# Optimization experiments

Hardware: AMD Instinct MI355X
Metric: run time of the kernel (lower is better)

Reference implementation:

```python
import jax, jax.numpy as jnp
import numpy as np

B, S, D = 2, 2048, 1024
H = 16
HD = D // H  # 64


def setup_inputs() -> dict:
    key = jax.random.key(0)
    ks = jax.random.split(key, 6)
    x = jax.random.normal(ks[0], (B, S, D), dtype=jnp.float32)
    sc = 1.0 / np.sqrt(D)
    Wq = jax.random.normal(ks[1], (D, D), dtype=jnp.float32) * sc
    Wk = jax.random.normal(ks[2], (D, D), dtype=jnp.float32) * sc
    Wv = jax.random.normal(ks[3], (D, D), dtype=jnp.float32) * sc
    Wo = jax.random.normal(ks[4], (D, D), dtype=jnp.float32) * sc
    bo = jax.random.normal(ks[5], (D,), dtype=jnp.float32) * 0.01
    return {"x": x, "Wq": Wq, "Wk": Wk, "Wv": Wv, "Wo": Wo, "bo": bo}


def reference(x, Wq, Wk, Wv, Wo, bo):
    b, s, d = x.shape
    # projections (torch Linear: y = x @ W.T; weights here stored as [d_in, d_out])
    Q = (x @ Wq).reshape(b, s, H, HD).transpose(0, 2, 1, 3)  # [b,h,s,hd]
    K = (x @ Wk).reshape(b, s, H, HD).transpose(0, 2, 1, 3)
    V = (x @ Wv).reshape(b, s, H, HD).transpose(0, 2, 1, 3)
    scores = jnp.einsum("bhqd,bhkd->bhqk", Q, K) / np.sqrt(HD)
    causal = jnp.triu(jnp.ones((s, s), dtype=bool), k=1)  # True above diagonal
    scores = jnp.where(causal[None, None], -jnp.inf, scores)
    attn = jax.nn.softmax(scores, axis=-1)
    # dropout_rate = 0.0 -> identity (eval-mode reference)
    ctx = jnp.einsum("bhqk,bhkd->bhqd", attn, V)
    ctx = ctx.transpose(0, 2, 1, 3).reshape(b, s, d)
    return ctx @ Wo + bo
```

## Files before the change

kernel.cpp:

```cpp
#include <hip/hip_runtime.h>
#include <hip/hip_bf16.h>

#define B_  2
#define S_  2048
#define D_  1024
#define H_  16
#define HD_ 64
#define M_  (B_*S_)

typedef __attribute__((ext_vector_type(8))) short short8;
typedef __attribute__((ext_vector_type(4))) float f32x4;

#define MFMA16(a, b, c) __builtin_amdgcn_mfma_f32_16x16x32_bf16((a), (b), (c), 0, 0, 0)

static __device__ inline short f2bf(float f) {
    union { float f; unsigned u; } v; v.f = f;
    unsigned r = v.u + 0x7FFFu + ((v.u >> 16) & 1u);
    return (short)(r >> 16);
}

static __device__ __forceinline__ float fexp2(float x) {
    float r;
    asm volatile("v_exp_f32 %0, %1\n\ts_nop 1" : "=v"(r) : "v"(x));
    return r;
}

static __device__ __forceinline__ unsigned cvt_pk_bf16(float lo, float hi) {
    unsigned r;
    asm volatile("v_cvt_pk_bf16_f32 %0, %1, %2" : "=v"(r) : "v"(lo), "v"(hi));
    return r;
}

static __device__ __forceinline__ void gl_lds16(const short* g, short* l) {
    __builtin_amdgcn_global_load_lds(
        (const __attribute__((address_space(1))) void*)g,
        (__attribute__((address_space(3))) void*)l, 16, 0, 0);
}

__global__ void prep_kernel(const float* __restrict__ x,
                            const float* __restrict__ Wq, const float* __restrict__ Wk,
                            const float* __restrict__ Wv, const float* __restrict__ Wo,
                            short* __restrict__ xb,
                            short* __restrict__ Wqkvt, short* __restrict__ Wot) {
    int z = blockIdx.z;
    if (z == 4) {
        int bid = blockIdx.y * 32 + blockIdx.x;
        int base = bid * 1024 + threadIdx.x;
#pragma unroll
        for (int it = 0; it < 4; ++it) {
            int i = base + it * 256;
            float4 v = ((const float4*)x)[i];
            short4 o;
            o.x = f2bf(v.x); o.y = f2bf(v.y); o.z = f2bf(v.z); o.w = f2bf(v.w);
            ((short4*)xb)[i] = o;
        }
        return;
    }
    __shared__ float tile[32][33];
    const float* W = (z == 0) ? Wq : (z == 1) ? Wk : (z == 2) ? Wv : Wo;
    short* Wt = (z == 3) ? Wot : (Wqkvt + ((size_t)z << 20));
    int tx = threadIdx.x & 31, ty = threadIdx.x >> 5;
    int n0 = blockIdx.x * 32, k0 = blockIdx.y * 32;
#pragma unroll
    for (int i = 0; i < 4; ++i)
        tile[ty + 8 * i][tx] = W[(size_t)(k0 + ty + 8 * i) * D_ + n0 + tx];
    __syncthreads();
#pragma unroll
    for (int i = 0; i < 4; ++i)
        Wt[(size_t)(n0 + ty + 8 * i) * D_ + k0 + tx] = f2bf(tile[tx][ty + 8 * i]);
}

__global__ __launch_bounds__(256) void gemm_qkv(const short* __restrict__ A,
                                                const short* __restrict__ Bt,
                                                short* __restrict__ out) {
    __shared__ __align__(16) short Asm[2][128 * 32];
    __shared__ __align__(16) short Bsm[2][128 * 32];
    const int NBX = 3;
    int X = blockIdx.x & 7, t = blockIdx.x >> 3;
    int bm = t / NBX, bn = X * NBX + t % NBX;
    int tid = threadIdx.x, l = tid & 63, w = tid >> 6;
    int lhi = l >> 4, llo = l & 15;
    int wm = w >> 1, wn = w & 1;

    f32x4 acc[4][4];
#pragma unroll
    for (int m = 0; m < 4; ++m)
#pragma unroll
        for (int n = 0; n < 4; ++n) acc[m][n] = (f32x4){0.f, 0.f, 0.f, 0.f};

    const short* Ag = A + (size_t)(bm * 128) * 1024;
    const short* Bg = Bt + (size_t)(bn * 128) * 1024;
    int c0 = tid, c1 = 256 + tid;
    int r0 = ((c0 >> 5) << 3) | (c0 & 7), s0 = ((c0 >> 3) & 3) ^ (r0 & 3);
    int r1 = ((c1 >> 5) << 3) | (c1 & 7), s1 = ((c1 >> 3) & 3) ^ (r1 & 3);

    auto stage = [&](int buf, int k0) {
        gl_lds16(Ag + (size_t)r0 * 1024 + k0 + s0 * 8, &Asm[buf][c0 * 8]);
        gl_lds16(Ag + (size_t)r1 * 1024 + k0 + s1 * 8, &Asm[buf][c1 * 8]);
        gl_lds16(Bg + (size_t)r0 * 1024 + k0 + s0 * 8, &Bsm[buf][c0 * 8]);
        gl_lds16(Bg + (size_t)r1 * 1024 + k0 + s1 * 8, &Bsm[buf][c1 * 8]);
    };

    int cia[4], cib[4];
#pragma unroll
    for (int m = 0; m < 4; ++m) {
        int row = wm * 64 + m * 16 + llo;
        cia[m] = ((row >> 3) << 5) | (((lhi ^ row) & 3) << 3) | (row & 7);
    }
#pragma unroll
    for (int n = 0; n < 4; ++n) {
        int row = wn * 64 + n * 16 + llo;
        cib[n] = ((row >> 3) << 5) | (((lhi ^ row) & 3) << 3) | (row & 7);
    }

    stage(0, 0);
    for (int i = 0; i < 32; ++i) {
        asm volatile("s_waitcnt vmcnt(0)" ::: "memory");
        __builtin_amdgcn_s_barrier();
        asm volatile("" ::: "memory");
        if (i + 1 < 32) stage((i + 1) & 1, (i + 1) * 32);
        int cur = i & 1;
        short8 af[4], bf[4];
#pragma unroll
        for (int m = 0; m < 4; ++m) af[m] = *(const short8*)&Asm[cur][cia[m] * 8];
#pragma unroll
        for (int n = 0; n < 4; ++n) bf[n] = *(const short8*)&Bsm[cur][cib[n] * 8];
#pragma unroll
        for (int m = 0; m < 4; ++m)
#pragma unroll
            for (int n = 0; n < 4; ++n)
                acc[m][n] = MFMA16(af[m], bf[n], acc[m][n]);
    }

    int rowb = bm * 128 + wm * 64, colb = bn * 128 + wn * 64;
#pragma unroll
    for (int m = 0; m < 4; ++m) {
#pragma unroll
        for (int n = 0; n < 4; ++n) {
            int col = colb + n * 16 + llo;
#pragma unroll
            for (int j = 0; j < 4; ++j) {
                int row = rowb + m * 16 + lhi * 4 + j;
                float v = acc[m][n][j];
                int proj = col >> 10, n1 = col & 1023;
                int h = n1 >> 6, hd = n1 & 63;
                int b = row >> 11, s = row & 2047;
                size_t off;
                if (proj == 0)
                    off = ((size_t)(b * 16 + h) * 2048 + s) * 64 + hd;
                else if (proj == 1)
                    off = (size_t)M_ * D_ + ((size_t)(b * 16 + h) * 2048 + s) * 64 + hd;
                else
                    off = (size_t)2 * M_ * D_ + ((size_t)(b * 16 + h) * 64 + hd) * 2048 + s;
                out[off] = f2bf(v);
            }
        }
    }
}

__global__ __launch_bounds__(256, 6) void gemm_out(const short* __restrict__ A,
                                                   const short* __restrict__ Bt,
                                                   const float* __restrict__ bias,
                                                   float* __restrict__ out) {
    __shared__ __align__(16) short Asm[2][64 * 32];
    __shared__ __align__(16) short Bsm[2][128 * 32];
    int bn = blockIdx.x & 7, bm = blockIdx.x >> 3;
    int tid = threadIdx.x, l = tid & 63, w = tid >> 6;
    int lhi = l >> 4, llo = l & 15;

    f32x4 acc[4][2];
#pragma unroll
    for (int m = 0; m < 4; ++m)
#pragma unroll
        for (int n = 0; n < 2; ++n) acc[m][n] = (f32x4){0.f, 0.f, 0.f, 0.f};

    const short* Ag = A + (size_t)(bm * 64) * 1024;
    const short* Bg = Bt + (size_t)(bn * 128) * 1024;
    int ca = tid;
    int ra = ((ca >> 5) << 3) | (ca & 7), sa = ((ca >> 3) & 3) ^ (ra & 3);
    int cb0 = tid, cb1 = tid + 256;
    int rb0 = ((cb0 >> 5) << 3) | (cb0 & 7), sb0 = ((cb0 >> 3) & 3) ^ (rb0 & 3);
    int rb1 = ((cb1 >> 5) << 3) | (cb1 & 7), sb1 = ((cb1 >> 3) & 3) ^ (rb1 & 3);

    auto stage = [&](int buf, int k0) {
        gl_lds16(Ag + (size_t)ra * 1024 + k0 + sa * 8, &Asm[buf][ca * 8]);
        gl_lds16(Bg + (size_t)rb0 * 1024 + k0 + sb0 * 8, &Bsm[buf][cb0 * 8]);
        gl_lds16(Bg + (size_t)rb1 * 1024 + k0 + sb1 * 8, &Bsm[buf][cb1 * 8]);
    };

    int cia[4], cib[2];
#pragma unroll
    for (int m = 0; m < 4; ++m) {
        int row = m * 16 + llo;
        cia[m] = ((row >> 3) << 5) | (((lhi ^ row) & 3) << 3) | (row & 7);
    }
#pragma unroll
    for (int n = 0; n < 2; ++n) {
        int row = w * 32 + n * 16 + llo;
        cib[n] = ((row >> 3) << 5) | (((lhi ^ row) & 3) << 3) | (row & 7);
    }

    stage(0, 0);
    for (int i = 0; i < 32; ++i) {
        asm volatile("s_waitcnt vmcnt(0)" ::: "memory");
        __builtin_amdgcn_s_barrier();
        asm volatile("" ::: "memory");
        if (i + 1 < 32) stage((i + 1) & 1, (i + 1) * 32);
        int cur = i & 1;
        short8 af[4], bf[2];
#pragma unroll
        for (int m = 0; m < 4; ++m) af[m] = *(const short8*)&Asm[cur][cia[m] * 8];
#pragma unroll
        for (int n = 0; n < 2; ++n) bf[n] = *(const short8*)&Bsm[cur][cib[n] * 8];
#pragma unroll
        for (int m = 0; m < 4; ++m)
#pragma unroll
            for (int n = 0; n < 2; ++n)
                acc[m][n] = MFMA16(af[m], bf[n], acc[m][n]);
    }

    int rowb = bm * 64, colb = bn * 128 + w * 32;
#pragma unroll
    for (int m = 0; m < 4; ++m)
#pragma unroll
        for (int n = 0; n < 2; ++n) {
            int col = colb + n * 16 + llo;
#pragma unroll
            for (int j = 0; j < 4; ++j) {
                int row = rowb + m * 16 + lhi * 4 + j;
                out[(size_t)row * 1024 + col] = acc[m][n][j] + bias[col];
            }
        }
}

__global__ __launch_bounds__(512) void attn_kernel(const short* __restrict__ Q,
                                                   const short* __restrict__ Kg,
                                                   const short* __restrict__ Vt,
                                                   short* __restrict__ ctx) {
    __shared__ __align__(16) char kvbuf[2][16384];
    __shared__ __align__(16) char plds[8][2048];
    int tid = threadIdx.x, w = tid >> 6, l = tid & 63;
    int lhi = l >> 4, llo = l & 15;
    int bh = blockIdx.x & 31, qp = blockIdx.x >> 5;
    int b = bh >> 4, h = bh & 15;
    char* pb = plds[w];

    const short* Qh = Q + (size_t)bh * S_ * HD_;
    const short* Kh = Kg + (size_t)bh * S_ * HD_;
    const short* Vh = Vt + (size_t)bh * HD_ * S_;

    int qbA = qp, qbB = 15 - qp;
    int NTA = 2 * qp + 2;
    const int NT = 34;

    int srow = tid >> 3;
    int ssrc = (16 * (tid & 7)) ^ ((srow & 7) << 4);
    auto stage = [&](char* buf, int c0) {
        gl_lds16(Kh + (size_t)(c0 + srow) * HD_ + (ssrc >> 1), (short*)(buf + tid * 16));
        gl_lds16(Vh + (size_t)srow * S_ + c0 + (ssrc >> 1), (short*)(buf + 8192 + tid * 16));
    };

    f32x4 O[4];
#pragma unroll
    for (int n = 0; n < 4; ++n) O[n] = (f32x4){0.f, 0.f, 0.f, 0.f};
    float lpart[4] = {0.f, 0.f, 0.f, 0.f};

    auto writeOut = [&](int qb) {
        int qbs = qb * 128 + w * 16;
#pragma unroll
        for (int j = 0; j < 4; ++j) {
            float ls = lpart[j];
            ls += __shfl_xor(ls, 1);
            ls += __shfl_xor(ls, 2);
            ls += __shfl_xor(ls, 4);
            ls += __shfl_xor(ls, 8);
            float inv = 1.0f / ls;
            int row = qbs + lhi * 4 + j;
            size_t base = ((size_t)(b * S_ + row)) * D_ + h * HD_;
#pragma unroll
            for (int n = 0; n < 4; ++n)
                ctx[base + n * 16 + llo] = f2bf(O[n][j] * inv);
        }
    };

    const float SC = 0.18033688f;
    const float M2 = 17.312340f;

    int qbase = qbA * 128 + w * 16;
    short8 aq0 = *(const short8*)(Qh + (size_t)(qbase + llo) * HD_ + 8 * lhi);
    short8 aq1 = *(const short8*)(Qh + (size_t)(qbase + llo) * HD_ + 32 + 8 * lhi);

    stage(kvbuf[0], 0);

    for (int i = 0; i < NT; ++i) {
        asm volatile("s_waitcnt vmcnt(0)" ::: "memory");
        __builtin_amdgcn_s_barrier();
        asm volatile("" ::: "memory");
        int kt = (i < NTA) ? i : i - NTA;
        int c0 = kt * 64;
        if (i + 1 < NT) {
            int ni = i + 1;
            int nkt = (ni < NTA) ? ni : ni - NTA;
            stage(kvbuf[ni & 1], nkt * 64);
        }
        const char* kb = kvbuf[i & 1];
        const char* vb = kb + 8192;

        if (c0 <= qbase + 15) {
            f32x4 sc4[4];
#pragma unroll
            for (int cb = 0; cb < 4; ++cb) {
                int row = cb * 16 + llo;
                int sw = (row & 7) << 4;
                short8 kf0 = *(const short8*)(kb + row * 128 + ((16 * lhi) ^ sw));
                short8 kf1 = *(const short8*)(kb + row * 128 + ((64 + 16 * lhi) ^ sw));
                f32x4 z = (f32x4){0.f, 0.f, 0.f, 0.f};
                z = MFMA16(aq0, kf0, z);
                z = MFMA16(aq1, kf1, z);
                sc4[cb] = z;
            }
            bool diag = (c0 + 63 > qbase);
#pragma unroll
            for (int j = 0; j < 4; ++j) {
                int qr = qbase + lhi * 4 + j;
                float v0 = fmaf(sc4[0][j], SC, -M2);
                float v1 = fmaf(sc4[1][j], SC, -M2);
                float v2 = fmaf(sc4[2][j], SC, -M2);
                float v3 = fmaf(sc4[3][j], SC, -M2);
                if (diag) {
                    if (c0 + llo > qr)      v0 = -1e30f;
                    if (c0 + 16 + llo > qr) v1 = -1e30f;
                    if (c0 + 32 + llo > qr) v2 = -1e30f;
                    if (c0 + 48 + llo > qr) v3 = -1e30f;
                }
                float p0 = fexp2(v0), p1 = fexp2(v1);
                float p2 = fexp2(v2), p3 = fexp2(v3);
                lpart[j] += (p0 + p1) + (p2 + p3);
                unsigned pk01 = cvt_pk_bf16(p0, p1);
                unsigned pk23 = cvt_pk_bf16(p2, p3);
                int r = lhi * 4 + j;
                char* rb = pb + r * 128;
                int sw = (r & 7) << 4;
                *(short*)(rb + ((2 * llo) ^ sw))      = (short)(pk01);
                *(short*)(rb + ((2 * llo + 32) ^ sw)) = (short)(pk01 >> 16);
                *(short*)(rb + ((2 * llo + 64) ^ sw)) = (short)(pk23);
                *(short*)(rb + ((2 * llo + 96) ^ sw)) = (short)(pk23 >> 16);
            }
            int swr = (llo & 7) << 4;
            short8 pa0 = *(const short8*)(pb + llo * 128 + ((16 * lhi) ^ swr));
            short8 pa1 = *(const short8*)(pb + llo * 128 + ((64 + 16 * lhi) ^ swr));
#pragma unroll
            for (int n = 0; n < 4; ++n) {
                int row = n * 16 + llo;
                int sw = (row & 7) << 4;
                short8 vf0 = *(const short8*)(vb + row * 128 + ((16 * lhi) ^ sw));
                short8 vf1 = *(const short8*)(vb + row * 128 + ((64 + 16 * lhi) ^ sw));
                O[n] = MFMA16(pa0, vf0, O[n]);
                O[n] = MFMA16(pa1, vf1, O[n]);
            }
        }

        if (i == NTA - 1) {
            writeOut(qbA);
#pragma unroll
            for (int n = 0; n < 4; ++n) O[n] = (f32x4){0.f, 0.f, 0.f, 0.f};
            lpart[0] = lpart[1] = lpart[2] = lpart[3] = 0.f;
            qbase = qbB * 128 + w * 16;
            aq0 = *(const short8*)(Qh + (size_t)(qbase + llo) * HD_ + 8 * lhi);
            aq1 = *(const short8*)(Qh + (size_t)(qbase + llo) * HD_ + 32 + 8 * lhi);
        }
    }
    writeOut(qbB);
}

extern "C" void kernel_launch(void* const* d_in, const int* in_sizes, int n_in,
                              void* d_out, int out_size, void* d_ws, size_t ws_size,
                              hipStream_t stream) {
    const float* x  = (const float*)d_in[0];
    const float* Wq = (const float*)d_in[1];
    const float* Wk = (const float*)d_in[2];
    const float* Wv = (const float*)d_in[3];
    const float* Wo = (const float*)d_in[4];
    const float* bo = (const float*)d_in[5];
    float* out = (float*)d_out;

    char* ws = (char*)d_ws;
    short* xb    = (short*)(ws);
    short* Wqkvt = (short*)(ws + (size_t)(8 << 20));
    short* Wot   = (short*)(ws + (size_t)(14 << 20));
    short* Qb    = (short*)(ws + (size_t)(16 << 20));
    short* Kb    = Qb + (size_t)M_ * D_;
    short* Vtb   = Qb + (size_t)2 * M_ * D_;
    short* ctx   = xb;

    prep_kernel<<<dim3(32, 32, 5), 256, 0, stream>>>(x, Wq, Wk, Wv, Wo, xb, Wqkvt, Wot);
    gemm_qkv<<<768, 256, 0, stream>>>(xb, Wqkvt, Qb);
    attn_kernel<<<256, 512, 0, stream>>>(Qb, Kb, Vtb, ctx);
    gemm_out<<<512, 256, 0, stream>>>(ctx, Wot, bo, out);
}
```

Measured before the change: 133.8 us.

## Rewrite QKV GEMM as 256x256-tile 8-wave ping-pong pipelined kernel

The QKV projection GEMM now uses 256x256 output tiles with 512 threads (8 waves), BK=64 and an 8-way XOR swizzle. It loads in halves across double buffers with fine-grained barriers, so that LDS reads, global-to-LDS staging and MFMA work interleave within each K step. The aim is fewer blocks (192), each with more reuse of A and B, and better overlap of memory traffic with matrix math. In exchange, register pressure rises (128 accumulator floats per lane) and there are many more barriers per iteration, which can limit occupancy.

```diff
diff --git a/kernel.cpp b/kernel.cpp
--- a/kernel.cpp
+++ b/kernel.cpp
@@ -70,78 +70,145 @@
         Wt[(size_t)(n0 + ty + 8 * i) * D_ + k0 + tx] = f2bf(tile[tx][ty + 8 * i]);
 }
 
-__global__ __launch_bounds__(256) void gemm_qkv(const short* __restrict__ A,
-                                                const short* __restrict__ Bt,
-                                                short* __restrict__ out) {
-    __shared__ __align__(16) short Asm[2][128 * 32];
-    __shared__ __align__(16) short Bsm[2][128 * 32];
-    const int NBX = 3;
-    int X = blockIdx.x & 7, t = blockIdx.x >> 3;
-    int bm = t / NBX, bn = X * NBX + t % NBX;
+__global__ __launch_bounds__(512) void gemm_qkv8p(const short* __restrict__ A,
+                                                  const short* __restrict__ Bt,
+                                                  short* __restrict__ out) {
+    __shared__ __align__(16) short lds[2][2][2][8192];
+    int wg = (blockIdx.x & 7) * 24 + (blockIdx.x >> 3);
+    int bn = wg / 16, bm = wg % 16;
     int tid = threadIdx.x, l = tid & 63, w = tid >> 6;
     int lhi = l >> 4, llo = l & 15;
-    int wm = w >> 1, wn = w & 1;
-
-    f32x4 acc[4][4];
-#pragma unroll
-    for (int m = 0; m < 4; ++m)
+    int wm = w >> 2, wn = w & 3;
+    int bh = wn >> 1;
+
+    f32x4 acc[8][4];
+#pragma unroll
+    for (int m = 0; m < 8; ++m)
 #pragma unroll
         for (int n = 0; n < 4; ++n) acc[m][n] = (f32x4){0.f, 0.f, 0.f, 0.f};
 
-    const short* Ag = A + (size_t)(bm * 128) * 1024;
-    const short* Bg = Bt + (size_t)(bn * 128) * 1024;
-    int c0 = tid, c1 = 256 + tid;
-    int r0 = ((c0 >> 5) << 3) | (c0 & 7), s0 = ((c0 >> 3) & 3) ^ (r0 & 3);
-    int r1 = ((c1 >> 5) << 3) | (c1 & 7), s1 = ((c1 >> 3) & 3) ^ (r1 & 3);
-
-    auto stage = [&](int buf, int k0) {
-        gl_lds16(Ag + (size_t)r0 * 1024 + k0 + s0 * 8, &Asm[buf][c0 * 8]);
-        gl_lds16(Ag + (size_t)r1 * 1024 + k0 + s1 * 8, &Asm[buf][c1 * 8]);
-        gl_lds16(Bg + (size_t)r0 * 1024 + k0 + s0 * 8, &Bsm[buf][c0 * 8]);
-        gl_lds16(Bg + (size_t)r1 * 1024 + k0 + s1 * 8, &Bsm[buf][c1 * 8]);
-    };
-
-    int cia[4], cib[4];
-#pragma unroll
-    for (int m = 0; m < 4; ++m) {
-        int row = wm * 64 + m * 16 + llo;
-        cia[m] = ((row >> 3) << 5) | (((lhi ^ row) & 3) << 3) | (row & 7);
-    }
-#pragma unroll
-    for (int n = 0; n < 4; ++n) {
-        int row = wn * 64 + n * 16 + llo;
-        cib[n] = ((row >> 3) << 5) | (((lhi ^ row) & 3) << 3) | (row & 7);
-    }
-
-    stage(0, 0);
-    for (int i = 0; i < 32; ++i) {
-        asm volatile("s_waitcnt vmcnt(0)" ::: "memory");
-        __builtin_amdgcn_s_barrier();
-        asm volatile("" ::: "memory");
-        if (i + 1 < 32) stage((i + 1) & 1, (i + 1) * 32);
-        int cur = i & 1;
-        short8 af[4], bf[4];
-#pragma unroll
-        for (int m = 0; m < 4; ++m) af[m] = *(const short8*)&Asm[cur][cia[m] * 8];
-#pragma unroll
-        for (int n = 0; n < 4; ++n) bf[n] = *(const short8*)&Bsm[cur][cib[n] * 8];
-#pragma unroll
-        for (int m = 0; m < 4; ++m)
-#pragma unroll
-            for (int n = 0; n < 4; ++n)
-                acc[m][n] = MFMA16(af[m], bf[n], acc[m][n]);
-    }
-
-    int rowb = bm * 128 + wm * 64, colb = bn * 128 + wn * 64;
-#pragma unroll
-    for (int m = 0; m < 4; ++m) {
+    const short* Ag = A + (size_t)(bm * 256) * 1024;
+    const short* Bg = Bt + (size_t)(bn * 256) * 1024;
+
+    int c0 = tid, c1 = tid + 512;
+    int ra0 = ((c0 >> 6) << 3) | (c0 & 7), sa0 = ((c0 >> 3) & 7) ^ (ra0 & 7);
+    int ra1 = ((c1 >> 6) << 3) | (c1 & 7), sa1 = ((c1 >> 3) & 7) ^ (ra1 & 7);
+
+    auto SA = [&](int buf, int half, int t) {
+        if (t >= 16) return;
+        gl_lds16(Ag + (size_t)(half * 128 + ra0) * 1024 + t * 64 + sa0 * 8,
+                 &lds[buf][0][half][c0 * 8]);
+        gl_lds16(Ag + (size_t)(half * 128 + ra1) * 1024 + t * 64 + sa1 * 8,
+                 &lds[buf][0][half][c1 * 8]);
+    };
+    auto SB = [&](int buf, int half, int t) {
+        if (t >= 16) return;
+        gl_lds16(Bg + (size_t)(half * 128 + ra0) * 1024 + t * 64 + sa0 * 8,
+                 &lds[buf][1][half][c0 * 8]);
+        gl_lds16(Bg + (size_t)(half * 128 + ra1) * 1024 + t * 64 + sa1 * 8,
+                 &lds[buf][1][half][c1 * 8]);
+    };
+
+    auto cidx = [](int row, int s) {
+        return ((row >> 3) << 6) | (((s ^ row) & 7) << 3) | (row & 7);
+    };
+    int cA[8][2], cB[4][2];
+#pragma unroll
+    for (int f = 0; f < 8; ++f)
+#pragma unroll
+        for (int kk = 0; kk < 2; ++kk)
+            cA[f][kk] = cidx(f * 16 + llo, kk * 4 + lhi);
+#pragma unroll
+    for (int n = 0; n < 4; ++n)
+#pragma unroll
+        for (int kk = 0; kk < 2; ++kk)
+            cB[n][kk] = cidx((wn & 1) * 64 + n * 16 + llo, kk * 4 + lhi);
+
+    short8 af[8], bfE[4], bfO[4];
+    auto LA = [&](int buf, int mh) {
+        const short* base = &lds[buf][0][wm][0];
+#pragma unroll
+        for (int mf = 0; mf < 4; ++mf)
+#pragma unroll
+            for (int kk = 0; kk < 2; ++kk)
+                af[mf * 2 + kk] = *(const short8*)&base[cA[mh * 4 + mf][kk] * 8];
+    };
+    auto LB = [&](short8* bf, int buf, int nh) {
+        const short* base = &lds[buf][1][bh][0];
+#pragma unroll
+        for (int nf = 0; nf < 2; ++nf)
+#pragma unroll
+            for (int kk = 0; kk < 2; ++kk)
+                bf[nf * 2 + kk] = *(const short8*)&base[cB[nh * 2 + nf][kk] * 8];
+    };
+    auto MQ = [&](const short8* bf, int mh, int nh) {
+#pragma unroll
+        for (int mf = 0; mf < 4; ++mf)
+#pragma unroll
+            for (int nf = 0; nf < 2; ++nf)
+#pragma unroll
+                for (int kk = 0; kk < 2; ++kk)
+                    acc[mh * 4 + mf][nh * 2 + nf] =
+                        MFMA16(af[mf * 2 + kk], bf[nf * 2 + kk],
+                               acc[mh * 4 + mf][nh * 2 + nf]);
+    };
+
+#define BARRIER() do { __builtin_amdgcn_s_barrier(); asm volatile("" ::: "memory"); } while (0)
+
+    SB(0, 0, 0); SB(0, 1, 0); SA(0, 0, 0); SA(0, 1, 0);
+    SB(1, 0, 1); SB(1, 1, 1);
+
+#pragma unroll 1
+    for (int it = 0; it < 8; ++it) {
+        int t1 = 2 * it + 1;
+        asm volatile("s_waitcnt vmcnt(4)" ::: "memory");
+        BARRIER();
+        LA(0, 0); LB(bfE, 0, 0);
+        SA(1, 0, t1);
+        MQ(bfE, 0, 0);
+        BARRIER();
+        LB(bfO, 0, 1);
+        SA(1, 1, t1);
+        MQ(bfO, 0, 1);
+        BARRIER();
+        LA(0, 1);
+        SB(0, 0, t1 + 1);
+        MQ(bfO, 1, 1);
+        BARRIER();
+        SB(0, 1, t1 + 1);
+        MQ(bfE, 1, 0);
+        BARRIER();
+        if (it == 7) { asm volatile("s_waitcnt vmcnt(0)" ::: "memory"); }
+        else         { asm volatile("s_waitcnt vmcnt(4)" ::: "memory"); }
+        BARRIER();
+        LA(1, 0); LB(bfE, 1, 0);
+        SA(0, 0, t1 + 1);
+        MQ(bfE, 0, 0);
+        BARRIER();
+        LB(bfO, 1, 1);
+        SA(0, 1, t1 + 1);
+        MQ(bfO, 0, 1);
+        BARRIER();
+        LA(1, 1);
+        SB(1, 0, t1 + 2);
+        MQ(bfO, 1, 1);
+        BARRIER();
+        SB(1, 1, t1 + 2);
+        MQ(bfE, 1, 0);
+        BARRIER();
+    }
+#undef BARRIER
+
+    int rowb = bm * 256 + wm * 128, colb = bn * 256 + wn * 64;
+#pragma unroll
+    for (int f = 0; f < 8; ++f) {
 #pragma unroll
         for (int n = 0; n < 4; ++n) {
             int col = colb + n * 16 + llo;
 #pragma unroll
             for (int j = 0; j < 4; ++j) {
-                int row = rowb + m * 16 + lhi * 4 + j;
-                float v = acc[m][n][j];
+                int row = rowb + f * 16 + lhi * 4 + j;
+                float v = acc[f][n][j];
                 int proj = col >> 10, n1 = col & 1023;
                 int h = n1 >> 6, hd = n1 & 63;
                 int b = row >> 11, s = row & 2047;
@@ -394,7 +461,7 @@
     short* ctx   = xb;
 
     prep_kernel<<<dim3(32, 32, 5), 256, 0, stream>>>(x, Wq, Wk, Wv, Wo, xb, Wqkvt, Wot);
-    gemm_qkv<<<768, 256, 0, stream>>>(xb, Wqkvt, Qb);
+    gemm_qkv8p<<<192, 512, 0, stream>>>(xb, Wqkvt, Qb);
     attn_kernel<<<256, 512, 0, stream>>>(Qb, Kb, Vtb, ctx);
     gemm_out<<<512, 256, 0, stream>>>(ctx, Wot, bo, out);
 }
```

Result: slower. 161.3 us (+20.6%).

## Double attention KV tile width to 128 keys per iteration

Applied to the files above, without the earlier changes.

Each loop iteration of the attention kernel now stages and processes 128 keys instead of 64, which halves the iteration count and the number of block-wide barriers and vmcnt waits. The K/V LDS buffers double to 32 KB each, and each wave gets two P staging buffers. The V tile uses a 256-byte row stride with a 16-way XOR swizzle. The cost is higher LDS use (about 96 KB per block), more registers for scores, and coarser causal skipping, so more masked work is done on diagonal tiles.

```diff
diff --git a/kernel.cpp b/kernel.cpp
--- a/kernel.cpp
+++ b/kernel.cpp
@@ -237,27 +237,33 @@
                                                    const short* __restrict__ Kg,
                                                    const short* __restrict__ Vt,
                                                    short* __restrict__ ctx) {
-    __shared__ __align__(16) char kvbuf[2][16384];
-    __shared__ __align__(16) char plds[8][2048];
+    __shared__ __align__(16) char kvbuf[2][32768];
+    __shared__ __align__(16) char plds[8][2][2048];
     int tid = threadIdx.x, w = tid >> 6, l = tid & 63;
     int lhi = l >> 4, llo = l & 15;
     int bh = blockIdx.x & 31, qp = blockIdx.x >> 5;
     int b = bh >> 4, h = bh & 15;
-    char* pb = plds[w];
+    char* pb0 = plds[w][0];
+    char* pb1 = plds[w][1];
 
     const short* Qh = Q + (size_t)bh * S_ * HD_;
     const short* Kh = Kg + (size_t)bh * S_ * HD_;
     const short* Vh = Vt + (size_t)bh * HD_ * S_;
 
     int qbA = qp, qbB = 15 - qp;
-    int NTA = 2 * qp + 2;
-    const int NT = 34;
-
-    int srow = tid >> 3;
-    int ssrc = (16 * (tid & 7)) ^ ((srow & 7) << 4);
+    int NTA = qp + 1;
+    const int NT = 17;
+
     auto stage = [&](char* buf, int c0) {
-        gl_lds16(Kh + (size_t)(c0 + srow) * HD_ + (ssrc >> 1), (short*)(buf + tid * 16));
-        gl_lds16(Vh + (size_t)srow * S_ + c0 + (ssrc >> 1), (short*)(buf + 8192 + tid * 16));
+#pragma unroll
+        for (int i2 = 0; i2 < 2; ++i2) {
+            int cc = tid + 512 * i2;
+            int kr = cc >> 3, ks = (16 * (cc & 7)) ^ ((kr & 7) << 4);
+            gl_lds16(Kh + (size_t)(c0 + kr) * HD_ + (ks >> 1), (short*)(buf + cc * 16));
+            int vr = cc >> 4, vs = (16 * (cc & 15)) ^ ((vr & 15) << 4);
+            gl_lds16(Vh + (size_t)vr * S_ + c0 + (vs >> 1),
+                     (short*)(buf + 16384 + cc * 16));
+        }
     };
 
     f32x4 O[4];
@@ -297,19 +303,19 @@
         __builtin_amdgcn_s_barrier();
         asm volatile("" ::: "memory");
         int kt = (i < NTA) ? i : i - NTA;
-        int c0 = kt * 64;
+        int c0 = kt * 128;
         if (i + 1 < NT) {
             int ni = i + 1;
             int nkt = (ni < NTA) ? ni : ni - NTA;
-            stage(kvbuf[ni & 1], nkt * 64);
+            stage(kvbuf[ni & 1], nkt * 128);
         }
         const char* kb = kvbuf[i & 1];
-        const char* vb = kb + 8192;
+        const char* vb = kb + 16384;
 
         if (c0 <= qbase + 15) {
-            f32x4 sc4[4];
-#pragma unroll
-            for (int cb = 0; cb < 4; ++cb) {
+            f32x4 sc4[8];
+#pragma unroll
+            for (int cb = 0; cb < 8; ++cb) {
                 int row = cb * 16 + llo;
                 int sw = (row & 7) << 4;
                 short8 kf0 = *(const short8*)(kb + row * 128 + ((16 * lhi) ^ sw));
@@ -319,44 +325,52 @@
                 z = MFMA16(aq1, kf1, z);
                 sc4[cb] = z;
             }
-            bool diag = (c0 + 63 > qbase);
+            bool diag = (c0 + 127 > qbase);
 #pragma unroll
             for (int j = 0; j < 4; ++j) {
                 int qr = qbase + lhi * 4 + j;
-                float v0 = fmaf(sc4[0][j], SC, -M2);
-                float v1 = fmaf(sc4[1][j], SC, -M2);
-                float v2 = fmaf(sc4[2][j], SC, -M2);
-                float v3 = fmaf(sc4[3][j], SC, -M2);
-                if (diag) {
-                    if (c0 + llo > qr)      v0 = -1e30f;
-                    if (c0 + 16 + llo > qr) v1 = -1e30f;
-                    if (c0 + 32 + llo > qr) v2 = -1e30f;
-                    if (c0 + 48 + llo > qr) v3 = -1e30f;
+                float p[8];
+#pragma unroll
+                for (int cb = 0; cb < 8; ++cb) {
+                    float v = fmaf(sc4[cb][j], SC, -M2);
+                    if (diag && (c0 + cb * 16 + llo > qr)) v = -1e30f;
+                    p[cb] = fexp2(v);
                 }
-                float p0 = fexp2(v0), p1 = fexp2(v1);
-                float p2 = fexp2(v2), p3 = fexp2(v3);
-                lpart[j] += (p0 + p1) + (p2 + p3);
-                unsigned pk01 = cvt_pk_bf16(p0, p1);
-                unsigned pk23 = cvt_pk_bf16(p2, p3);
+                lpart[j] += ((p[0] + p[1]) + (p[2] + p[3])) +
+                            ((p[4] + p[5]) + (p[6] + p[7]));
                 int r = lhi * 4 + j;
-                char* rb = pb + r * 128;
                 int sw = (r & 7) << 4;
-                *(short*)(rb + ((2 * llo) ^ sw))      = (short)(pk01);
-                *(short*)(rb + ((2 * llo + 32) ^ sw)) = (short)(pk01 >> 16);
-                *(short*)(rb + ((2 * llo + 64) ^ sw)) = (short)(pk23);
-                *(short*)(rb + ((2 * llo + 96) ^ sw)) = (short)(pk23 >> 16);
+                unsigned pkA = cvt_pk_bf16(p[0], p[1]);
+                unsigned pkB = cvt_pk_bf16(p[2], p[3]);
+                char* rb = pb0 + r * 128;
+                *(short*)(rb + ((2 * llo) ^ sw))      = (short)(pkA);
+                *(short*)(rb + ((2 * llo + 32) ^ sw)) = (short)(pkA >> 16);
+                *(short*)(rb + ((2 * llo + 64) ^ sw)) = (short)(pkB);
+                *(short*)(rb + ((2 * llo + 96) ^ sw)) = (short)(pkB >> 16);
+                unsigned pkC = cvt_pk_bf16(p[4], p[5]);
+                unsigned pkD = cvt_pk_bf16(p[6], p[7]);
+                rb = pb1 + r * 128;
+                *(short*)(rb + ((2 * llo) ^ sw))      = (short)(pkC);
+                *(short*)(rb + ((2 * llo + 32) ^ sw)) = (short)(pkC >> 16);
+                *(short*)(rb + ((2 * llo + 64) ^ sw)) = (short)(pkD);
+                *(short*)(rb + ((2 * llo + 96) ^ sw)) = (short)(pkD >> 16);
             }
             int swr = (llo & 7) << 4;
-            short8 pa0 = *(const short8*)(pb + llo * 128 + ((16 * lhi) ^ swr));
-            short8 pa1 = *(const short8*)(pb + llo * 128 + ((64 + 16 * lhi) ^ swr));
+            short8 pa[4];
+            pa[0] = *(const short8*)(pb0 + llo * 128 + ((16 * lhi) ^ swr));
+            pa[1] = *(const short8*)(pb0 + llo * 128 + ((64 + 16 * lhi) ^ swr));
+            pa[2] = *(const short8*)(pb1 + llo * 128 + ((16 * lhi) ^ swr));
+            pa[3] = *(const short8*)(pb1 + llo * 128 + ((64 + 16 * lhi) ^ swr));
 #pragma unroll
             for (int n = 0; n < 4; ++n) {
-                int row = n * 16 + llo;
-                int sw = (row & 7) << 4;
-                short8 vf0 = *(const short8*)(vb + row * 128 + ((16 * lhi) ^ sw));
-                short8 vf1 = *(const short8*)(vb + row * 128 + ((64 + 16 * lhi) ^ sw));
-                O[n] = MFMA16(pa0, vf0, O[n]);
-                O[n] = MFMA16(pa1, vf1, O[n]);
+                int vrow = n * 16 + llo;
+                int vsw = (vrow & 15) << 4;
+#pragma unroll
+                for (int kc = 0; kc < 4; ++kc) {
+                    short8 vf = *(const short8*)(vb + vrow * 256 +
+                                                 ((kc * 64 + 16 * lhi) ^ vsw));
+                    O[n] = MFMA16(pa[kc], vf, O[n]);
+                }
             }
         }
 
```

After: 130.0 us. -2.9%, faster.
